# Optimization experiments

Hardware: AMD Instinct MI355X
Metric: run time of the kernel (lower is better)

The kernel has to match this reference:

```python
import jax, jax.numpy as jnp
import numpy as np

B, S, DIM = 2, 2048, 2048
H, DH = 16, 128            # head_dim = dim // n_heads; decop_rot_dim == head_dim (required by the view)
LKV, LQ = 512, 1024        # latent kv / q compression dims


def setup_inputs() -> dict:
    key = jax.random.key(0)
    ks = jax.random.split(key, 12)
    w = lambda k, shape: jax.random.normal(k, shape, jnp.float32) * 0.02
    x = jax.random.normal(ks[0], (B, S, DIM), jnp.float32)
    # rotary table: angles[t, i] = t * 10000^(-2i/DH), complex passed as cos/sin pair
    inv_freq = 1.0 / (10000.0 ** (np.arange(0, DH, 2, dtype=np.float64) / DH))
    ang = np.outer(np.arange(S, dtype=np.float64), inv_freq)  # [S, DH/2]
    return {
        "x": x,
        "freq_cos": jnp.asarray(np.cos(ang), jnp.float32),
        "freq_sin": jnp.asarray(np.sin(ang), jnp.float32),
        "w_lq": w(ks[1], (LQ, DIM)),
        "w_lkv": w(ks[2], (LKV, DIM)),
        "w_q": w(ks[3], (H * DH, LQ)),
        "w_k": w(ks[4], (H * DH, LKV)),
        "w_v": w(ks[5], (H * DH, LKV)),
        "w_qr": w(ks[6], (H * DH, LQ)),
        "b_qr": w(ks[7], (H * DH,)),
        "w_kr": w(ks[8], (H * DH, DIM)),
        "b_kr": w(ks[9], (H * DH,)),
        "w_o": w(ks[10], (DIM, H * DH)),
        "b_o": w(ks[11], (DIM,)),
    }


def _rope(t, freq):
    # t: [B,S,H,DH]; freq: [S,DH/2] complex. Pairs (even,odd) along last dim rotated.
    b, s, h, d = t.shape
    tc = t.astype(jnp.float32).reshape(b, s, h, d // 2, 2)
    tc = jax.lax.complex(tc[..., 0], tc[..., 1]) * freq[None, :, None, :]
    return jnp.stack([jnp.real(tc), jnp.imag(tc)], axis=-1).reshape(b, s, h, d).astype(t.dtype)


def reference(x, freq_cos, freq_sin, w_lq, w_lkv, w_q, w_k, w_v, w_qr, b_qr, w_kr, b_kr, w_o, b_o):
    b, s, _ = x.shape
    freq = jax.lax.complex(freq_cos, freq_sin)          # [S, DH/2]
    cq = x @ w_lq.T                                      # [B,S,LQ]
    ckv = x @ w_lkv.T                                    # [B,S,LKV]
    q = (cq @ w_q.T).reshape(b, s, H, DH)
    qr = _rope((cq @ w_qr.T + b_qr).reshape(b, s, H, DH), freq)
    k = (ckv @ w_k.T).reshape(b, s, H, DH)
    kr = _rope((x @ w_kr.T + b_kr).reshape(b, s, H, DH), freq)
    v = (ckv @ w_v.T).reshape(b, s, H, DH)
    q = jnp.concatenate([q, qr], axis=-1)                # [B,S,H,2*DH]
    k = jnp.concatenate([k, kr], axis=-1)
    # note: scale uses sqrt(head_dim), NOT sqrt(2*head_dim), faithful to source
    scores = jnp.einsum('bqhd,bkhd->bhqk', q, k) / jnp.sqrt(jnp.float32(DH))
    att = jax.nn.softmax(scores.astype(jnp.float32), axis=-1).astype(q.dtype)
    out = jnp.einsum('bhqk,bkhd->bqhd', att, v).reshape(b, s, H * DH)
    return out @ w_o.T + b_o
```

## Files before the change

kernel.cpp:

```cpp
#include <hip/hip_runtime.h>
#include <hip/hip_bf16.h>


#define Bb 2
#define Ss 2048
#define DIMd 2048
#define Hh 16
#define DHd 128

typedef __hip_bfloat16 bf16;
typedef __attribute__((ext_vector_type(8))) short short8;
typedef __attribute__((ext_vector_type(4))) float floatx4;
typedef __attribute__((ext_vector_type(16))) float floatx16;

#define MFMA(a, b, c) __builtin_amdgcn_mfma_f32_16x16x32_bf16((a), (b), (c), 0, 0, 0)
#define MFMA32(a, b, c) __builtin_amdgcn_mfma_f32_32x32x16_bf16((a), (b), (c), 0, 0, 0)

__device__ __forceinline__ void async16(const bf16* g, bf16* l) {
  __builtin_amdgcn_global_load_lds(
      (const __attribute__((address_space(1))) unsigned int*)g,
      (__attribute__((address_space(3))) unsigned int*)l, 16, 0, 0);
}

__global__ __launch_bounds__(256) void cvt_all(
    const float* x, const float* wlq, const float* wlkv, const float* wq,
    const float* wqr, const float* wk, const float* wv, const float* wkr,
    const float* wo, bf16* dx, bf16* dwlq, bf16* dwlkv, bf16* dwq, bf16* dwqr,
    bf16* dwk, bf16* dwv, bf16* dwkr, bf16* dwo) {
  long i = (long)blockIdx.x * 256 + threadIdx.x;
  const float* src;
  bf16* dst;
  long base;
  if (i < 2097152L)      { src = x;    dst = dx;    base = 0; }
  else if (i < 2621440L) { src = wlq;  dst = dwlq;  base = 2097152L; }
  else if (i < 2883584L) { src = wlkv; dst = dwlkv; base = 2621440L; }
  else if (i < 3407872L) { src = wq;   dst = dwq;   base = 2883584L; }
  else if (i < 3932160L) { src = wqr;  dst = dwqr;  base = 3407872L; }
  else if (i < 4194304L) { src = wk;   dst = dwk;   base = 3932160L; }
  else if (i < 4456448L) { src = wv;   dst = dwv;   base = 4194304L; }
  else if (i < 5505024L) { src = wkr;  dst = dwkr;  base = 4456448L; }
  else                   { src = wo;   dst = dwo;   base = 5505024L; }
  long j = i - base;
  float4 f = ((const float4*)src)[j];
  union { ushort4 u4; bf16 h[4]; } cv;
  cv.h[0] = __float2bfloat16(f.x);
  cv.h[1] = __float2bfloat16(f.y);
  cv.h[2] = __float2bfloat16(f.z);
  cv.h[3] = __float2bfloat16(f.w);
  ((ushort4*)dst)[j] = cv.u4;
}

template <int MODE>
__device__ __forceinline__ void gemm_body(const bf16* __restrict__ A,
                                          const bf16* __restrict__ Bw,
                                          const float* __restrict__ bias,
                                          void* __restrict__ Cout,
                                          void* __restrict__ Cout2,
                                          const float* __restrict__ fco,
                                          const float* __restrict__ fsi,
                                          int M, int N, int K, int lda) {
  extern __shared__ __align__(16) bf16 smem[];
  bf16* As = smem;
  bf16* Bs = smem + 8192;
  const int tid = threadIdx.x;
  const int lane = tid & 63;
  const int w = tid >> 6;
  const int wm = w & 1, wn = w >> 1;
  const int m0 = blockIdx.y * 128, n0 = blockIdx.x * 128;
  const int lr = lane & 15, lg = lane >> 4;

  floatx4 acc[4][4];
#pragma unroll
  for (int mi = 0; mi < 4; ++mi)
#pragma unroll
    for (int ni = 0; ni < 4; ++ni)
#pragma unroll
      for (int r = 0; r < 4; ++r) acc[mi][ni][r] = 0.f;

  for (int k0 = 0; k0 < K; k0 += 64) {
    __syncthreads();
#pragma unroll
    for (int i = 0; i < 4; ++i) {
      int c = i * 256 + tid;
      int row = c >> 3;
      int cg = (c & 7) ^ (row & 7);
      async16(A + (size_t)(m0 + row) * lda + k0 + cg * 8, As + (i * 256 + w * 64) * 8);
      async16(Bw + (size_t)(n0 + row) * K + k0 + cg * 8, Bs + (i * 256 + w * 64) * 8);
    }
    __syncthreads();

#pragma unroll
    for (int ks = 0; ks < 2; ++ks) {
      short8 af[4], bfr[4];
#pragma unroll
      for (int mi = 0; mi < 4; ++mi) {
        int row = wm * 64 + mi * 16 + lr;
        af[mi] = *(const short8*)&As[row * 64 + (((ks * 4 + lg) ^ (lr & 7)) * 8)];
      }
#pragma unroll
      for (int ni = 0; ni < 4; ++ni) {
        int row = wn * 64 + ni * 16 + lr;
        bfr[ni] = *(const short8*)&Bs[row * 64 + (((ks * 4 + lg) ^ (lr & 7)) * 8)];
      }
#pragma unroll
      for (int mi = 0; mi < 4; ++mi)
#pragma unroll
        for (int ni = 0; ni < 4; ++ni)
          acc[mi][ni] = MFMA(af[mi], bfr[ni], acc[mi][ni]);
    }
  }

  if (MODE == 5 && n0 >= 2048) {
    __syncthreads();
#pragma unroll
    for (int mi = 0; mi < 4; ++mi)
#pragma unroll
      for (int ni = 0; ni < 4; ++ni)
#pragma unroll
        for (int r = 0; r < 4; ++r) {
          int ml = wm * 64 + mi * 16 + lg * 4 + r;
          int nl = wn * 64 + ni * 16 + lr;
          smem[ml * 129 + nl] = __float2bfloat16(acc[mi][ni][r]);
        }
    __syncthreads();
    int bb = m0 >> 11, s0 = m0 & 2047;
    int hh = (n0 - 2048) >> 7;
    short* vbase = (short*)Cout2 + ((size_t)(bb * Hh + hh) * 128) * Ss;
#pragma unroll
    for (int pa = 0; pa < 8; ++pa) {
      int d = pa * 16 + (tid >> 4);
      int sc = (tid & 15) * 8;
      short8 v;
#pragma unroll
      for (int i = 0; i < 8; ++i) v[i] = *(const short*)&smem[(sc + i) * 129 + d];
      *(short8*)(vbase + (size_t)d * Ss + s0 + sc) = v;
    }
    return;
  }

#pragma unroll
  for (int mi = 0; mi < 4; ++mi)
#pragma unroll
    for (int ni = 0; ni < 4; ++ni)
#pragma unroll
      for (int r = 0; r < 4; ++r) {
        int m = m0 + wm * 64 + mi * 16 + lg * 4 + r;
        int n = n0 + wn * 64 + ni * 16 + lr;
        float v = acc[mi][ni][r];
        int bb = m >> 11, s = m & 2047;
        if (MODE == 3) {
          v += bias[n];
          ((float*)Cout)[(size_t)m * N + n] = v;
        } else if (MODE == 4) {
          if (n < 2048) {
            int hh = n >> 7, d = n & 127;
            ((bf16*)Cout)[((size_t)((bb * Hh + hh) * Ss + s)) * 256 + d] =
                __float2bfloat16(v);
          } else {
            int n2 = n - 2048;
            int hh = n2 >> 7, d = n2 & 127;
            v += bias[n2];
            float vp = __shfl_xor(v, 1, 64);
            float co = fco[s * 64 + (d >> 1)];
            float sn = fsi[s * 64 + (d >> 1)];
            v = (d & 1) ? (v * co + vp * sn) : (v * co - vp * sn);
            ((bf16*)Cout)[((size_t)((bb * Hh + hh) * Ss + s)) * 256 + 128 + d] =
                __float2bfloat16(v);
          }
        } else if (MODE == 5) {
          int hh = n >> 7, d = n & 127;
          ((bf16*)Cout)[((size_t)((bb * Hh + hh) * Ss + s)) * 256 + d] =
              __float2bfloat16(v);
        } else if (MODE == 6) {
          if (n < 1536) {
            ((bf16*)Cout)[(size_t)m * 1536 + n] = __float2bfloat16(v);
          } else {
            int n2 = n - 1536;
            int hh = n2 >> 7, d = n2 & 127;
            v += bias[n2];
            float vp = __shfl_xor(v, 1, 64);
            float co = fco[s * 64 + (d >> 1)];
            float sn = fsi[s * 64 + (d >> 1)];
            v = (d & 1) ? (v * co + vp * sn) : (v * co - vp * sn);
            ((bf16*)Cout2)[((size_t)((bb * Hh + hh) * Ss + s)) * 256 + 128 + d] =
                __float2bfloat16(v);
          }
        }
      }
}

template <int MODE>
__global__ __launch_bounds__(256, 4) void gemm_bt(const bf16* __restrict__ A,
                                                  const bf16* __restrict__ Bw,
                                                  const float* __restrict__ bias,
                                                  void* __restrict__ Cout,
                                                  void* __restrict__ Cout2,
                                                  const float* __restrict__ fco,
                                                  const float* __restrict__ fsi,
                                                  int M, int N, int K, int lda) {
  gemm_body<MODE>(A, Bw, bias, Cout, Cout2, fco, fsi, M, N, K, lda);
}

__global__ __launch_bounds__(256, 4) void gemm_qkv(const bf16* __restrict__ ccat,
                                                   const bf16* __restrict__ wqcat,
                                                   const bf16* __restrict__ wkvcat,
                                                   const float* __restrict__ bqr,
                                                   void* __restrict__ qcat,
                                                   void* __restrict__ kcat,
                                                   void* __restrict__ vt,
                                                   const float* __restrict__ fco,
                                                   const float* __restrict__ fsi) {
  if (blockIdx.z == 0)
    gemm_body<4>(ccat, wqcat, bqr, qcat, nullptr, fco, fsi, 4096, 4096, 1024, 1536);
  else
    gemm_body<5>(ccat + 1024, wkvcat, nullptr, kcat, vt, nullptr, nullptr, 4096, 4096, 512, 1536);
}

__global__ __launch_bounds__(256, 2) void flash_attn(const bf16* __restrict__ Q,
                                                     const bf16* __restrict__ Kc,
                                                     const bf16* __restrict__ Vt,
                                                     bf16* __restrict__ Oa) {
  const float CE = 0.08838834764831845f * 1.4426950408889634f;
  __shared__ __align__(16) bf16 Ks[64 * 256];
  __shared__ __align__(16) bf16 Vs[128 * 64];

  const int lane = threadIdx.x & 63;
  const int w = threadIdx.x >> 6;
  const int m = lane & 31;
  const int hi = lane >> 5;
  const int bh = blockIdx.x;
  const int b = bh >> 4, h = bh & 15;
  const int q0 = blockIdx.y * 128 + w * 32;

  const bf16* Qb = Q + (size_t)bh * Ss * 256;
  const bf16* Kb = Kc + (size_t)bh * Ss * 256;
  const bf16* Vb = Vt + (size_t)bh * 128 * Ss;

  short8 qf[16];
  {
    const short* Qrow = (const short*)Qb + (size_t)(q0 + m) * 256 + hi * 8;
#pragma unroll
    for (int dt = 0; dt < 16; ++dt) qf[dt] = *(const short8*)(Qrow + dt * 16);
  }

  const int key = m & 7;
  const short* kp[2][4];
#pragma unroll
  for (int cbt = 0; cbt < 2; ++cbt)
#pragma unroll
    for (int dl = 0; dl < 4; ++dl)
      kp[cbt][dl] = (const short*)Ks + (cbt * 32 + m) * 256 + (((2 * dl + hi) ^ key) * 8);
  const short* vp[4];
#pragma unroll
  for (int kb = 0; kb < 4; ++kb)
    vp[kb] = (const short*)Vs + m * 64 + (((2 * kb + hi) ^ key) * 8);

  float l = 0.f;
  floatx16 oacc[4];
#pragma unroll
  for (int nb = 0; nb < 4; ++nb)
#pragma unroll
    for (int r = 0; r < 16; ++r) oacc[nb][r] = 0.f;

  const bool lo = (lane < 32);

  for (int j0 = 0; j0 < Ss; j0 += 64) {
    __syncthreads();
#pragma unroll
    for (int i = 0; i < 8; ++i) {
      int r = w * 16 + i * 2 + (lane >> 5);
      int cg = (lane & 31) ^ (r & 7);
      async16(Kb + (size_t)(j0 + r) * 256 + cg * 8, Ks + (w * 16 + i * 2) * 256);
    }
#pragma unroll
    for (int i = 0; i < 4; ++i) {
      int r = w * 32 + i * 8 + (lane >> 3);
      int cg = (lane & 7) ^ (r & 7);
      async16(Vb + (size_t)r * Ss + j0 + cg * 8, Vs + (w * 32 + i * 8) * 64);
    }
    __syncthreads();

    floatx16 sf[2];
#pragma unroll
    for (int t = 0; t < 2; ++t)
#pragma unroll
      for (int r = 0; r < 16; ++r) sf[t][r] = 0.f;
#pragma unroll
    for (int cbt = 0; cbt < 2; ++cbt)
#pragma unroll
      for (int dt = 0; dt < 16; ++dt) {
        short8 kf = *(const short8*)(kp[cbt][dt & 3] + (dt >> 2) * 64);
        sf[cbt] = MFMA32(kf, qf[dt], sf[cbt]);
      }

    unsigned pk[2][8];
#pragma unroll
    for (int t = 0; t < 2; ++t)
#pragma unroll
      for (int rp = 0; rp < 8; ++rp) {
        float p0 = exp2f(sf[t][2 * rp] * CE);
        float p1 = exp2f(sf[t][2 * rp + 1] * CE);
        l += p0 + p1;
        bf16 b0 = __float2bfloat16(p0);
        bf16 b1 = __float2bfloat16(p1);
        pk[t][rp] = ((unsigned)*(const unsigned short*)&b1 << 16) |
                    *(const unsigned short*)&b0;
      }

#pragma unroll
    for (int kb = 0; kb < 4; ++kb) {
      const int t = kb >> 1, b4 = (kb & 1) * 4;
      unsigned x1 = lo ? pk[t][b4 + 2] : pk[t][b4];
      unsigned y1 = (unsigned)__shfl_xor((int)x1, 32, 64);
      unsigned x2 = lo ? pk[t][b4 + 3] : pk[t][b4 + 1];
      unsigned y2 = (unsigned)__shfl_xor((int)x2, 32, 64);
      union { unsigned u[4]; short8 s; } pa;
      pa.u[0] = lo ? pk[t][b4] : y1;
      pa.u[1] = lo ? pk[t][b4 + 1] : y2;
      pa.u[2] = lo ? y1 : pk[t][b4 + 2];
      pa.u[3] = lo ? y2 : pk[t][b4 + 3];
#pragma unroll
      for (int nb = 0; nb < 4; ++nb) {
        short8 vf = *(const short8*)(vp[kb] + nb * 2048);
        oacc[nb] = MFMA32(pa.s, vf, oacc[nb]);
      }
    }
  }

  float lsum = l + __shfl_xor(l, 32, 64);
  float inv = 1.f / lsum;

#pragma unroll
  for (int r = 0; r < 16; ++r) {
    int qr = (r & 3) + 8 * (r >> 2) + 4 * hi;
    float invr = __shfl(inv, (lane & 32) + qr, 64);
    int s = q0 + qr;
#pragma unroll
    for (int nb = 0; nb < 4; ++nb) {
      int d = nb * 32 + m;
      Oa[((size_t)(b * Ss + s)) * (Hh * 128) + h * 128 + d] =
          __float2bfloat16(oacc[nb][r] * invr);
    }
  }
}

extern "C" void kernel_launch(void* const* d_in, const int* in_sizes, int n_in,
                              void* d_out, int out_size, void* d_ws, size_t ws_size,
                              hipStream_t stream) {
  const float* x    = (const float*)d_in[0];
  const float* fco  = (const float*)d_in[1];
  const float* fsi  = (const float*)d_in[2];
  const float* wlq  = (const float*)d_in[3];
  const float* wlkv = (const float*)d_in[4];
  const float* wq   = (const float*)d_in[5];
  const float* wk   = (const float*)d_in[6];
  const float* wv   = (const float*)d_in[7];
  const float* wqr  = (const float*)d_in[8];
  const float* bqr  = (const float*)d_in[9];
  const float* wkr  = (const float*)d_in[10];
  const float* bkr  = (const float*)d_in[11];
  const float* wo   = (const float*)d_in[12];
  const float* bo   = (const float*)d_in[13];

  char* ws = (char*)d_ws;
  size_t o = 0;
  bf16* x_b    = (bf16*)(ws + o); o += (size_t)Bb * Ss * DIMd * 2;
  bf16* wbig   = (bf16*)(ws + o); o += (size_t)3584 * 2048 * 2;
  bf16* wqcat  = (bf16*)(ws + o); o += (size_t)4096 * 1024 * 2;
  bf16* wkvcat = (bf16*)(ws + o); o += (size_t)4096 * 512 * 2;
  bf16* wo_b   = (bf16*)(ws + o); o += (size_t)2048 * 2048 * 2;
  bf16* ccat   = (bf16*)(ws + o); o += (size_t)4096 * 1536 * 2;
  bf16* qcat   = (bf16*)(ws + o); o += (size_t)Bb * Hh * Ss * 256 * 2;
  bf16* kcat   = (bf16*)(ws + o); o += (size_t)Bb * Hh * Ss * 256 * 2;
  bf16* vt     = (bf16*)(ws + o); o += (size_t)Bb * Hh * 128 * Ss * 2;
  bf16* attn   = (bf16*)(ws + o); o += (size_t)4096 * 2048 * 2;

  cvt_all<<<25600, 256, 0, stream>>>(
      x, wlq, wlkv, wq, wqr, wk, wv, wkr, wo,
      x_b,
      wbig,
      wbig + (size_t)1024 * 2048,
      wqcat,
      wqcat + (size_t)2048 * 1024,
      wkvcat,
      wkvcat + (size_t)2048 * 512,
      wbig + (size_t)1536 * 2048,
      wo_b);

  const int M = Bb * Ss;
  const int GEMM_LDS = 128 * 129 * 2;
  gemm_bt<6><<<dim3(28, 32), 256, GEMM_LDS, stream>>>(
      x_b, wbig, bkr, ccat, kcat, fco, fsi, M, 3584, 2048, 2048);
  gemm_qkv<<<dim3(32, 32, 2), 256, GEMM_LDS, stream>>>(
      ccat, wqcat, wkvcat, bqr, qcat, kcat, vt, fco, fsi);

  flash_attn<<<dim3(Bb * Hh, Ss / 128), 256, 0, stream>>>(qcat, kcat, vt, attn);

  gemm_bt<3><<<dim3(16, 32), 256, GEMM_LDS, stream>>>(
      attn, wo_b, bo, (float*)d_out, nullptr, nullptr, nullptr, M, 2048, 2048, 2048);
}
```

Before: 459.4 us.

## Double-buffer flash attention K/V tiles with 32-key stages and permlane swaps

Replaces the single 64-key K/V LDS tile with two 32-key buffers so the async global-to-LDS load of the next tile overlaps the MFMA work on the current one, with one barrier per stage. It also swaps the shfl_xor plus select P-matrix exchange for permlane32_swap and adds s_setprio around the MFMA blocks. The cost is smaller per-stage tiles, more barriers overall, and a different V swizzle that has to stay consistent with the read pattern.

```diff
diff --git a/kernel.cpp b/kernel.cpp
--- a/kernel.cpp
+++ b/kernel.cpp
@@ -12,6 +12,7 @@
 typedef __attribute__((ext_vector_type(8))) short short8;
 typedef __attribute__((ext_vector_type(4))) float floatx4;
 typedef __attribute__((ext_vector_type(16))) float floatx16;
+typedef __attribute__((ext_vector_type(2))) unsigned int uintx2;
 
 #define MFMA(a, b, c) __builtin_amdgcn_mfma_f32_16x16x32_bf16((a), (b), (c), 0, 0, 0)
 #define MFMA32(a, b, c) __builtin_amdgcn_mfma_f32_32x32x16_bf16((a), (b), (c), 0, 0, 0)
@@ -216,13 +217,66 @@
     gemm_body<5>(ccat + 1024, wkvcat, nullptr, kcat, vt, nullptr, nullptr, 4096, 4096, 512, 1536);
 }
 
+#define FA_STAGE(KSN, VSN, J)                                                    \
+  {                                                                              \
+    _Pragma("unroll") for (int i = 0; i < 4; ++i) {                              \
+      int r = w * 8 + i * 2 + (lane >> 5);                                       \
+      async16(Kb + (size_t)((J) + r) * 256 + (((lane & 31) ^ (r & 7)) * 8),      \
+              KSN + (w * 8 + i * 2) * 256);                                      \
+    }                                                                            \
+    _Pragma("unroll") for (int i = 0; i < 2; ++i) {                              \
+      int d = w * 32 + i * 16 + (lane >> 2);                                     \
+      async16(Vb + (size_t)d * Ss + (J) + (((lane & 3) ^ ((d >> 1) & 3)) * 8),   \
+              VSN + (w * 32 + i * 16) * 32);                                     \
+    }                                                                            \
+  }
+
+#define FA_COMPUTE(KP, VQ)                                                       \
+  {                                                                              \
+    floatx16 sf;                                                                 \
+    _Pragma("unroll") for (int r = 0; r < 16; ++r) sf[r] = 0.f;                  \
+    __builtin_amdgcn_s_setprio(1);                                               \
+    _Pragma("unroll") for (int dt = 0; dt < 16; ++dt) {                          \
+      short8 kf = *(const short8*)(KP[dt & 3] + (dt >> 2) * 64);                 \
+      sf = MFMA32(kf, qf[dt], sf);                                               \
+    }                                                                            \
+    __builtin_amdgcn_s_setprio(0);                                               \
+    unsigned pk[8];                                                              \
+    _Pragma("unroll") for (int rp = 0; rp < 8; ++rp) {                           \
+      float p0 = exp2f(sf[2 * rp] * CE);                                         \
+      float p1 = exp2f(sf[2 * rp + 1] * CE);                                     \
+      l += p0 + p1;                                                              \
+      bf16 b0 = __float2bfloat16(p0);                                            \
+      bf16 b1 = __float2bfloat16(p1);                                            \
+      pk[rp] = ((unsigned)*(const unsigned short*)&b1 << 16) |                   \
+               *(const unsigned short*)&b0;                                      \
+    }                                                                            \
+    __builtin_amdgcn_s_setprio(1);                                               \
+    _Pragma("unroll") for (int kb = 0; kb < 2; ++kb) {                           \
+      uintx2 w02 = __builtin_amdgcn_permlane32_swap(pk[kb * 4 + 0],              \
+                                                    pk[kb * 4 + 2], false, false); \
+      uintx2 w13 = __builtin_amdgcn_permlane32_swap(pk[kb * 4 + 1],              \
+                                                    pk[kb * 4 + 3], false, false); \
+      union { unsigned u[4]; short8 s; } pa;                                     \
+      pa.u[0] = w02.x; pa.u[1] = w13.x; pa.u[2] = w02.y; pa.u[3] = w13.y;        \
+      _Pragma("unroll") for (int nb = 0; nb < 4; ++nb) {                         \
+        short8 vf = *(const short8*)(VQ[kb] + nb * 1024);                        \
+        oacc[nb] = MFMA32(pa.s, vf, oacc[nb]);                                   \
+      }                                                                          \
+    }                                                                            \
+    __builtin_amdgcn_s_setprio(0);                                               \
+    __syncthreads();                                                             \
+  }
+
 __global__ __launch_bounds__(256, 2) void flash_attn(const bf16* __restrict__ Q,
                                                      const bf16* __restrict__ Kc,
                                                      const bf16* __restrict__ Vt,
                                                      bf16* __restrict__ Oa) {
   const float CE = 0.08838834764831845f * 1.4426950408889634f;
-  __shared__ __align__(16) bf16 Ks[64 * 256];
-  __shared__ __align__(16) bf16 Vs[128 * 64];
+  __shared__ __align__(16) bf16 Ks0[32 * 256];
+  __shared__ __align__(16) bf16 Ks1[32 * 256];
+  __shared__ __align__(16) bf16 Vs0[128 * 32];
+  __shared__ __align__(16) bf16 Vs1[128 * 32];
 
   const int lane = threadIdx.x & 63;
   const int w = threadIdx.x >> 6;
@@ -244,16 +298,23 @@
   }
 
   const int key = m & 7;
-  const short* kp[2][4];
-#pragma unroll
-  for (int cbt = 0; cbt < 2; ++cbt)
-#pragma unroll
-    for (int dl = 0; dl < 4; ++dl)
-      kp[cbt][dl] = (const short*)Ks + (cbt * 32 + m) * 256 + (((2 * dl + hi) ^ key) * 8);
-  const short* vp[4];
-#pragma unroll
-  for (int kb = 0; kb < 4; ++kb)
-    vp[kb] = (const short*)Vs + m * 64 + (((2 * kb + hi) ^ key) * 8);
+  const int vkey = (m >> 1) & 3;
+  const short* kp0[4];
+  const short* kp1[4];
+#pragma unroll
+  for (int dl = 0; dl < 4; ++dl) {
+    int off = m * 256 + (((2 * dl + hi) ^ key) * 8);
+    kp0[dl] = (const short*)Ks0 + off;
+    kp1[dl] = (const short*)Ks1 + off;
+  }
+  const short* vq0[2];
+  const short* vq1[2];
+#pragma unroll
+  for (int kb = 0; kb < 2; ++kb) {
+    int off = m * 32 + (((2 * kb + hi) ^ vkey) * 8);
+    vq0[kb] = (const short*)Vs0 + off;
+    vq1[kb] = (const short*)Vs1 + off;
+  }
 
   float l = 0.f;
   floatx16 oacc[4];
@@ -262,69 +323,16 @@
 #pragma unroll
     for (int r = 0; r < 16; ++r) oacc[nb][r] = 0.f;
 
-  const bool lo = (lane < 32);
-
-  for (int j0 = 0; j0 < Ss; j0 += 64) {
-    __syncthreads();
-#pragma unroll
-    for (int i = 0; i < 8; ++i) {
-      int r = w * 16 + i * 2 + (lane >> 5);
-      int cg = (lane & 31) ^ (r & 7);
-      async16(Kb + (size_t)(j0 + r) * 256 + cg * 8, Ks + (w * 16 + i * 2) * 256);
-    }
-#pragma unroll
-    for (int i = 0; i < 4; ++i) {
-      int r = w * 32 + i * 8 + (lane >> 3);
-      int cg = (lane & 7) ^ (r & 7);
-      async16(Vb + (size_t)r * Ss + j0 + cg * 8, Vs + (w * 32 + i * 8) * 64);
-    }
-    __syncthreads();
-
-    floatx16 sf[2];
-#pragma unroll
-    for (int t = 0; t < 2; ++t)
-#pragma unroll
-      for (int r = 0; r < 16; ++r) sf[t][r] = 0.f;
-#pragma unroll
-    for (int cbt = 0; cbt < 2; ++cbt)
-#pragma unroll
-      for (int dt = 0; dt < 16; ++dt) {
-        short8 kf = *(const short8*)(kp[cbt][dt & 3] + (dt >> 2) * 64);
-        sf[cbt] = MFMA32(kf, qf[dt], sf[cbt]);
-      }
-
-    unsigned pk[2][8];
-#pragma unroll
-    for (int t = 0; t < 2; ++t)
-#pragma unroll
-      for (int rp = 0; rp < 8; ++rp) {
-        float p0 = exp2f(sf[t][2 * rp] * CE);
-        float p1 = exp2f(sf[t][2 * rp + 1] * CE);
-        l += p0 + p1;
-        bf16 b0 = __float2bfloat16(p0);
-        bf16 b1 = __float2bfloat16(p1);
-        pk[t][rp] = ((unsigned)*(const unsigned short*)&b1 << 16) |
-                    *(const unsigned short*)&b0;
-      }
-
-#pragma unroll
-    for (int kb = 0; kb < 4; ++kb) {
-      const int t = kb >> 1, b4 = (kb & 1) * 4;
-      unsigned x1 = lo ? pk[t][b4 + 2] : pk[t][b4];
-      unsigned y1 = (unsigned)__shfl_xor((int)x1, 32, 64);
-      unsigned x2 = lo ? pk[t][b4 + 3] : pk[t][b4 + 1];
-      unsigned y2 = (unsigned)__shfl_xor((int)x2, 32, 64);
-      union { unsigned u[4]; short8 s; } pa;
-      pa.u[0] = lo ? pk[t][b4] : y1;
-      pa.u[1] = lo ? pk[t][b4 + 1] : y2;
-      pa.u[2] = lo ? y1 : pk[t][b4 + 2];
-      pa.u[3] = lo ? y2 : pk[t][b4 + 3];
-#pragma unroll
-      for (int nb = 0; nb < 4; ++nb) {
-        short8 vf = *(const short8*)(vp[kb] + nb * 2048);
-        oacc[nb] = MFMA32(pa.s, vf, oacc[nb]);
-      }
-    }
+  FA_STAGE(Ks0, Vs0, 0);
+  __syncthreads();
+
+#pragma unroll 1
+  for (int g = 0; g < 64; g += 2) {
+    FA_STAGE(Ks1, Vs1, (g + 1) * 32);
+    FA_COMPUTE(kp0, vq0);
+    int jn = (g + 2) * 32;
+    if (jn < Ss) FA_STAGE(Ks0, Vs0, jn);
+    FA_COMPUTE(kp1, vq1);
   }
 
   float lsum = l + __shfl_xor(l, 32, 64);
```

New measurement: 457.4 us. About the same (-0.4%).
